# Optimization experiments

Hardware: AMD Instinct MI355X
Metric: run time of the kernel (lower is better)

## Reference

```python
import jax, jax.numpy as jnp
import numpy as np

B, H, S, D = 4, 16, 2048, 64
INV_SCALE_FACTOR = 8.0  # scores are divided by this (== sqrt(D))
DROPOUT_P = 0.0         # deterministic baseline; dropout is identity at p=0


def setup_inputs() -> dict:
    key = jax.random.key(0)
    kq, kk, kv = jax.random.split(key, 3)
    return {
        "query": jax.random.normal(kq, (B, H, S, D), dtype=jnp.float32),
        "key": jax.random.normal(kk, (B, H, S, D), dtype=jnp.float32),
        "value": jax.random.normal(kv, (B, H, S, D), dtype=jnp.float32),
    }


def reference(query, key, value):
    # scores: [B, H, Sq, Sk]
    scores = jnp.einsum("bhqd,bhkd->bhqk", query, key) / INV_SCALE_FACTOR
    probs = jax.nn.softmax(scores, axis=-1)
    # dropout_p == 0.0 -> identity
    out = jnp.einsum("bhqk,bhkd->bhqd", probs, value)
    return out
```

## Files before the change

kernel.cpp:

```cpp
#include <hip/hip_runtime.h>


#define S_LEN 2048
#define D_DIM 64
#define TK    64
#define NTILE (S_LEN / TK)
#define LOG2E_OVER8 0.18033688011112042f
#define VTILE (64 * 64)
#define VBH   (NTILE * VTILE)

typedef __bf16 bf16x8 __attribute__((ext_vector_type(8)));
typedef short  s16x4  __attribute__((ext_vector_type(4)));
typedef float  f32x4  __attribute__((ext_vector_type(4)));
typedef unsigned short us;

__device__ __forceinline__ us f2bf(float f) {
    union { __bf16 h; us u; } c;
    c.h = (__bf16)f;
    return c.u;
}

__device__ __forceinline__ unsigned pk2(float a, float b) {
#if __has_builtin(__builtin_amdgcn_cvt_pk_bf16_f32)
    typedef __bf16 bf2 __attribute__((ext_vector_type(2)));
    union { bf2 h; unsigned u; } c;
    c.h = __builtin_amdgcn_cvt_pk_bf16_f32(a, b);
    return c.u;
#else
    return ((unsigned)f2bf(b) << 16) | f2bf(a);
#endif
}

__device__ __forceinline__ float fast_exp2(float x) {
#if __has_builtin(__builtin_amdgcn_exp2f)
    return __builtin_amdgcn_exp2f(x);
#else
    return exp2f(x);
#endif
}

__device__ __forceinline__ void gload_lds16(const void* g, void* l) {
    __builtin_amdgcn_global_load_lds(
        (const __attribute__((address_space(1))) unsigned int*)g,
        (__attribute__((address_space(3))) unsigned int*)l, 16, 0, 0);
}

__device__ __forceinline__ f32x4 mfma16x16x16(s16x4 a, s16x4 b, f32x4 c) {
#if __has_builtin(__builtin_amdgcn_mfma_f32_16x16x16bf16_1k)
    return __builtin_amdgcn_mfma_f32_16x16x16bf16_1k(a, b, c, 0, 0, 0);
#else
    f32x4 d = c;
    asm volatile("v_mfma_f32_16x16x16_bf16 %0, %1, %2, %0"
                 : "+v"(d) : "v"(a), "v"(b));
    return d;
#endif
}

__global__ __launch_bounds__(256)
void prep(const float* __restrict__ K, const float* __restrict__ V,
          us* __restrict__ Kb, us* __restrict__ Vt) {
    __shared__ us Ls[64 * 68];
    const int bx = blockIdx.x, tid = threadIdx.x;
    if (bx < 4096) {
        const size_t i = ((size_t)bx * 256 + tid) * 8;
        const float4 a = *(const float4*)(K + i);
        const float4 b = *(const float4*)(K + i + 4);
        union { us u[8]; uint4 q; } pk;
        pk.u[0] = f2bf(a.x); pk.u[1] = f2bf(a.y);
        pk.u[2] = f2bf(a.z); pk.u[3] = f2bf(a.w);
        pk.u[4] = f2bf(b.x); pk.u[5] = f2bf(b.y);
        pk.u[6] = f2bf(b.z); pk.u[7] = f2bf(b.w);
        *(uint4*)(Kb + i) = pk.q;
    } else {
        const int idx = bx - 4096;
        const int t = idx & (NTILE - 1), bh = idx >> 5;
        {
            const int r = tid >> 2, seg = tid & 3;
            const float* src = V + ((size_t)bh * S_LEN + t * TK + r) * D_DIM + seg * 16;
            us* dst = &Ls[r * 68 + seg * 16];
#pragma unroll
            for (int i = 0; i < 2; ++i) {
                const float4 v0 = *(const float4*)(src + 8 * i);
                const float4 v1 = *(const float4*)(src + 8 * i + 4);
                union { us u[8]; uint2 q[2]; } pk;
                pk.u[0] = f2bf(v0.x); pk.u[1] = f2bf(v0.y);
                pk.u[2] = f2bf(v0.z); pk.u[3] = f2bf(v0.w);
                pk.u[4] = f2bf(v1.x); pk.u[5] = f2bf(v1.y);
                pk.u[6] = f2bf(v1.z); pk.u[7] = f2bf(v1.w);
                *(uint2*)(dst + 8 * i) = pk.q[0];
                *(uint2*)(dst + 8 * i + 4) = pk.q[1];
            }
        }
        __syncthreads();
        {
            const int lane = tid & 63, db = tid >> 6;
            const int quad = lane >> 4, l15 = lane & 15;
            const int d = db * 16 + l15;
            us* dst = Vt + (size_t)bh * VBH + t * VTILE + lane * 8;
#pragma unroll
            for (int c = 0; c < 2; ++c) {
                union { us u[8]; uint4 q; } pk;
#pragma unroll
                for (int e = 0; e < 8; ++e) {
                    const int k = (2 * c + (e >> 2)) * 16 + quad * 4 + (e & 3);
                    pk.u[e] = Ls[k * 68 + d];
                }
                *(uint4*)(dst + (c * 4 + db) * 512) = pk.q;
            }
        }
    }
}

__global__ __launch_bounds__(256, 4)
void fa_fwd(const float* __restrict__ Qg, const us* __restrict__ Kb,
            const us* __restrict__ Vtb, float* __restrict__ Og) {
    __shared__ __align__(16) us Kl[2][TK * 64];

    const int tid  = threadIdx.x;
    const int w    = tid >> 6;
    const int lane = tid & 63;
    const int l15  = lane & 15;
    const int quad = lane >> 4;
    const int x    = l15 & 7;

    const int bid   = blockIdx.x;
    const int chunk = bid >> 3;
    const int bh    = ((bid & 7) << 3) | (chunk >> 4);
    const int qb    = chunk & 15;
    const size_t base = (size_t)bh * S_LEN * D_DIM;

    bf16x8 bq00, bq01, bq10, bq11;
    {
        const float* q0 = Qg + base + (size_t)(qb * 128 + w * 32 + l15) * D_DIM + quad * 8;
        const float* q1 = q0 + 16 * D_DIM;
#define LOADQ(dst0, dst1, p)                                                  \
        {                                                                     \
            const float4 x0 = *(const float4*)(p);                            \
            const float4 x1 = *(const float4*)((p) + 4);                      \
            const float4 y0 = *(const float4*)((p) + 32);                     \
            const float4 y1 = *(const float4*)((p) + 36);                     \
            dst0[0]=(__bf16)(x0.x*LOG2E_OVER8); dst0[1]=(__bf16)(x0.y*LOG2E_OVER8); \
            dst0[2]=(__bf16)(x0.z*LOG2E_OVER8); dst0[3]=(__bf16)(x0.w*LOG2E_OVER8); \
            dst0[4]=(__bf16)(x1.x*LOG2E_OVER8); dst0[5]=(__bf16)(x1.y*LOG2E_OVER8); \
            dst0[6]=(__bf16)(x1.z*LOG2E_OVER8); dst0[7]=(__bf16)(x1.w*LOG2E_OVER8); \
            dst1[0]=(__bf16)(y0.x*LOG2E_OVER8); dst1[1]=(__bf16)(y0.y*LOG2E_OVER8); \
            dst1[2]=(__bf16)(y0.z*LOG2E_OVER8); dst1[3]=(__bf16)(y0.w*LOG2E_OVER8); \
            dst1[4]=(__bf16)(y1.x*LOG2E_OVER8); dst1[5]=(__bf16)(y1.y*LOG2E_OVER8); \
            dst1[6]=(__bf16)(y1.z*LOG2E_OVER8); dst1[7]=(__bf16)(y1.w*LOG2E_OVER8); \
        }
        LOADQ(bq00, bq01, q0)
        LOADQ(bq10, bq11, q1)
#undef LOADQ
    }

    const int krow   = w * 16 + (lane >> 3);
    const int kchunk = (lane & 7) ^ (lane >> 3);
    const us* ksrc = Kb + base + (size_t)krow * D_DIM + kchunk * 8;
    const us* vg0 = Vtb + (size_t)bh * VBH + lane * 8;

    float lv0 = 0.f, lv1 = 0.f;
    f32x4 oa0[4], oa1[4];
#pragma unroll
    for (int db = 0; db < 4; ++db) {
        oa0[db] = (f32x4){0.f, 0.f, 0.f, 0.f};
        oa1[db] = (f32x4){0.f, 0.f, 0.f, 0.f};
    }

#pragma unroll
    for (int j = 0; j < 2; ++j)
        gload_lds16(ksrc + j * 512, &Kl[0][w * 1024 + j * 512]);
    __syncthreads();

    s16x4 bus0[4], bus1[4];

#define QK_STEP(kb)                                                            \
    {                                                                          \
        const int row_ = (kb) * 16 + l15;                                      \
        const bf16x8 a0 = *(const bf16x8*)&kl[row_ * 64 + ((quad ^ x) * 8)];   \
        const bf16x8 a1 = *(const bf16x8*)&kl[row_ * 64 + (((4 + quad) ^ x) * 8)]; \
        f32x4 c0 = {0.f, 0.f, 0.f, 0.f};                                       \
        c0 = __builtin_amdgcn_mfma_f32_16x16x32_bf16(a0, bq00, c0, 0, 0, 0);   \
        c0 = __builtin_amdgcn_mfma_f32_16x16x32_bf16(a1, bq01, c0, 0, 0, 0);   \
        f32x4 c1 = {0.f, 0.f, 0.f, 0.f};                                       \
        c1 = __builtin_amdgcn_mfma_f32_16x16x32_bf16(a0, bq10, c1, 0, 0, 0);   \
        c1 = __builtin_amdgcn_mfma_f32_16x16x32_bf16(a1, bq11, c1, 0, 0, 0);   \
        const float p00 = fast_exp2(c0[0]), p01 = fast_exp2(c0[1]);            \
        const float p02 = fast_exp2(c0[2]), p03 = fast_exp2(c0[3]);            \
        lv0 += (p00 + p01) + (p02 + p03);                                      \
        const float p10 = fast_exp2(c1[0]), p11 = fast_exp2(c1[1]);            \
        const float p12 = fast_exp2(c1[2]), p13 = fast_exp2(c1[3]);            \
        lv1 += (p10 + p11) + (p12 + p13);                                      \
        union { unsigned u[2]; s16x4 s; } b0_, b1_;                            \
        b0_.u[0] = pk2(p00, p01); b0_.u[1] = pk2(p02, p03);                    \
        b1_.u[0] = pk2(p10, p11); b1_.u[1] = pk2(p12, p13);                    \
        bus0[kb] = b0_.s; bus1[kb] = b1_.s;                                    \
    }

#define PV_PAIR(K0)                                                            \
    _Pragma("unroll")                                                          \
    for (int db = 0; db < 4; ++db) {                                           \
        union { uint4 q; s16x4 s[2]; } va;                                     \
        va.q = vqa[db];                                                        \
        oa0[db] = mfma16x16x16(va.s[0], bus0[K0], oa0[db]);                    \
        oa1[db] = mfma16x16x16(va.s[0], bus1[K0], oa1[db]);                    \
        oa0[db] = mfma16x16x16(va.s[1], bus0[(K0) + 1], oa0[db]);              \
        oa1[db] = mfma16x16x16(va.s[1], bus1[(K0) + 1], oa1[db]);              \
    }

#pragma unroll 1
    for (int t = 0; t < NTILE; ++t) {
        const int cur = t & 1;
        const us* kl = Kl[cur];
        const us* vg = vg0 + (size_t)t * VTILE;

        uint4 vqa[4];
#pragma unroll
        for (int f = 0; f < 4; ++f) vqa[f] = *(const uint4*)(vg + f * 512);

        QK_STEP(0)
        QK_STEP(1)
        PV_PAIR(0)

#pragma unroll
        for (int f = 0; f < 4; ++f) vqa[f] = *(const uint4*)(vg + (4 + f) * 512);

        if (t + 1 < NTILE) {
            const us* ks = ksrc + (size_t)(t + 1) * (TK * D_DIM);
            us* kd = &Kl[cur ^ 1][w * 1024];
#pragma unroll
            for (int j = 0; j < 2; ++j)
                gload_lds16(ks + j * 512, kd + j * 512);
        }

        QK_STEP(2)
        QK_STEP(3)
        PV_PAIR(2)

        __syncthreads();
    }
#undef QK_STEP
#undef PV_PAIR

    float lq0 = lv0;
    lq0 += __shfl_xor(lq0, 16, 64);
    lq0 += __shfl_xor(lq0, 32, 64);
    float lq1 = lv1;
    lq1 += __shfl_xor(lq1, 16, 64);
    lq1 += __shfl_xor(lq1, 32, 64);
    const float inv0 = 1.f / lq0;
    const float inv1 = 1.f / lq1;
    float* op0 = Og + base + (size_t)(qb * 128 + w * 32 + l15) * D_DIM + quad * 4;
    float* op1 = op0 + 16 * D_DIM;
#pragma unroll
    for (int db = 0; db < 4; ++db) {
        float4 v0 = { oa0[db][0] * inv0, oa0[db][1] * inv0,
                      oa0[db][2] * inv0, oa0[db][3] * inv0 };
        *(float4*)(op0 + db * 16) = v0;
        float4 v1 = { oa1[db][0] * inv1, oa1[db][1] * inv1,
                      oa1[db][2] * inv1, oa1[db][3] * inv1 };
        *(float4*)(op1 + db * 16) = v1;
    }
}

extern "C" void kernel_launch(void* const* d_in, const int* in_sizes, int n_in,
                              void* d_out, int out_size, void* d_ws, size_t ws_size,
                              hipStream_t stream) {
    const float* Q = (const float*)d_in[0];
    const float* K = (const float*)d_in[1];
    const float* V = (const float*)d_in[2];
    float* O = (float*)d_out;

    us* Kb = (us*)d_ws;
    us* Vt = Kb + (size_t)64 * S_LEN * D_DIM;

    prep<<<4096 + 2048, 256, 0, stream>>>(K, V, Kb, Vt);
    fa_fwd<<<dim3(1024), 256, 0, stream>>>(Q, Kb, Vt, O);
}
```

Baseline: 212.6 us.

## Software-pipeline QK of next tile with PV of current tile

Restructures the main loop so the QK^T/exp step for tile t+1 is computed while the PV MFMAs for tile t run, using two ping-pong probability register sets and prefetching K two tiles ahead. A prologue computes tile 0 scores and an epilogue finishes the last PV. The aim is to interleave the exp/pack ALU work with MFMA work and hide LDS latency, at the cost of more live registers, which may lower occupancy.

```diff
diff --git a/kernel.cpp b/kernel.cpp
--- a/kernel.cpp
+++ b/kernel.cpp
@@ -166,18 +166,13 @@
         oa1[db] = (f32x4){0.f, 0.f, 0.f, 0.f};
     }
 
-#pragma unroll
-    for (int j = 0; j < 2; ++j)
-        gload_lds16(ksrc + j * 512, &Kl[0][w * 1024 + j * 512]);
-    __syncthreads();
-
-    s16x4 bus0[4], bus1[4];
-
-#define QK_STEP(kb)                                                            \
+    s16x4 busA0[4], busA1[4], busB0[4], busB1[4];
+
+#define QK_STEP(KL, kb, B0, B1)                                                \
     {                                                                          \
         const int row_ = (kb) * 16 + l15;                                      \
-        const bf16x8 a0 = *(const bf16x8*)&kl[row_ * 64 + ((quad ^ x) * 8)];   \
-        const bf16x8 a1 = *(const bf16x8*)&kl[row_ * 64 + (((4 + quad) ^ x) * 8)]; \
+        const bf16x8 a0 = *(const bf16x8*)&(KL)[row_ * 64 + ((quad ^ x) * 8)]; \
+        const bf16x8 a1 = *(const bf16x8*)&(KL)[row_ * 64 + (((4 + quad) ^ x) * 8)]; \
         f32x4 c0 = {0.f, 0.f, 0.f, 0.f};                                       \
         c0 = __builtin_amdgcn_mfma_f32_16x16x32_bf16(a0, bq00, c0, 0, 0, 0);   \
         c0 = __builtin_amdgcn_mfma_f32_16x16x32_bf16(a1, bq01, c0, 0, 0, 0);   \
@@ -193,53 +188,78 @@
         union { unsigned u[2]; s16x4 s; } b0_, b1_;                            \
         b0_.u[0] = pk2(p00, p01); b0_.u[1] = pk2(p02, p03);                    \
         b1_.u[0] = pk2(p10, p11); b1_.u[1] = pk2(p12, p13);                    \
-        bus0[kb] = b0_.s; bus1[kb] = b1_.s;                                    \
-    }
-
-#define PV_PAIR(K0)                                                            \
+        (B0)[kb] = b0_.s; (B1)[kb] = b1_.s;                                    \
+    }
+
+#define PV_PAIR(VQA, B0, B1, K0)                                               \
     _Pragma("unroll")                                                          \
     for (int db = 0; db < 4; ++db) {                                           \
         union { uint4 q; s16x4 s[2]; } va;                                     \
-        va.q = vqa[db];                                                        \
-        oa0[db] = mfma16x16x16(va.s[0], bus0[K0], oa0[db]);                    \
-        oa1[db] = mfma16x16x16(va.s[0], bus1[K0], oa1[db]);                    \
-        oa0[db] = mfma16x16x16(va.s[1], bus0[(K0) + 1], oa0[db]);              \
-        oa1[db] = mfma16x16x16(va.s[1], bus1[(K0) + 1], oa1[db]);              \
-    }
+        va.q = (VQA)[db];                                                      \
+        oa0[db] = mfma16x16x16(va.s[0], (B0)[K0], oa0[db]);                    \
+        oa1[db] = mfma16x16x16(va.s[0], (B1)[K0], oa1[db]);                    \
+        oa0[db] = mfma16x16x16(va.s[1], (B0)[(K0) + 1], oa0[db]);              \
+        oa1[db] = mfma16x16x16(va.s[1], (B1)[(K0) + 1], oa1[db]);              \
+    }
+
+#define TILE_BODY(T, BU0, BU1, BB0, BB1, KLN, KLPF, DOPF)                      \
+    {                                                                          \
+        __syncthreads();                                                       \
+        const us* vg = vg0 + (size_t)(T) * VTILE;                              \
+        uint4 vqa[4];                                                          \
+        _Pragma("unroll")                                                      \
+        for (int f = 0; f < 4; ++f) vqa[f] = *(const uint4*)(vg + f * 512);    \
+        QK_STEP(KLN, 0, BB0, BB1)                                              \
+        QK_STEP(KLN, 1, BB0, BB1)                                              \
+        PV_PAIR(vqa, BU0, BU1, 0)                                              \
+        _Pragma("unroll")                                                      \
+        for (int f = 0; f < 4; ++f) vqa[f] = *(const uint4*)(vg + (4 + f) * 512); \
+        if (DOPF) {                                                            \
+            const us* ks_ = ksrc + (size_t)((T) + 2) * (TK * D_DIM);           \
+            us* kd_ = &(KLPF)[w * 1024];                                       \
+            gload_lds16(ks_, kd_);                                             \
+            gload_lds16(ks_ + 512, kd_ + 512);                                 \
+        }                                                                      \
+        QK_STEP(KLN, 2, BB0, BB1)                                              \
+        QK_STEP(KLN, 3, BB0, BB1)                                              \
+        PV_PAIR(vqa, BU0, BU1, 2)                                              \
+    }
+
+    gload_lds16(ksrc, &Kl[0][w * 1024]);
+    gload_lds16(ksrc + 512, &Kl[0][w * 1024 + 512]);
+    __syncthreads();
+    {
+        const us* ks_ = ksrc + (size_t)(TK * D_DIM);
+        us* kd_ = &Kl[1][w * 1024];
+        gload_lds16(ks_, kd_);
+        gload_lds16(ks_ + 512, kd_ + 512);
+    }
+    QK_STEP(Kl[0], 0, busA0, busA1)
+    QK_STEP(Kl[0], 1, busA0, busA1)
+    QK_STEP(Kl[0], 2, busA0, busA1)
+    QK_STEP(Kl[0], 3, busA0, busA1)
 
 #pragma unroll 1
-    for (int t = 0; t < NTILE; ++t) {
-        const int cur = t & 1;
-        const us* kl = Kl[cur];
-        const us* vg = vg0 + (size_t)t * VTILE;
-
+    for (int it = 0; it < 15; ++it) {
+        const int t0 = it * 2;
+        TILE_BODY(t0,     busA0, busA1, busB0, busB1, Kl[1], Kl[0], 1)
+        TILE_BODY(t0 + 1, busB0, busB1, busA0, busA1, Kl[0], Kl[1], 1)
+    }
+    TILE_BODY(30, busA0, busA1, busB0, busB1, Kl[1], Kl[0], 0)
+
+    {
+        const us* vg = vg0 + (size_t)31 * VTILE;
         uint4 vqa[4];
 #pragma unroll
         for (int f = 0; f < 4; ++f) vqa[f] = *(const uint4*)(vg + f * 512);
-
-        QK_STEP(0)
-        QK_STEP(1)
-        PV_PAIR(0)
-
+        PV_PAIR(vqa, busB0, busB1, 0)
 #pragma unroll
         for (int f = 0; f < 4; ++f) vqa[f] = *(const uint4*)(vg + (4 + f) * 512);
-
-        if (t + 1 < NTILE) {
-            const us* ks = ksrc + (size_t)(t + 1) * (TK * D_DIM);
-            us* kd = &Kl[cur ^ 1][w * 1024];
-#pragma unroll
-            for (int j = 0; j < 2; ++j)
-                gload_lds16(ks + j * 512, kd + j * 512);
-        }
-
-        QK_STEP(2)
-        QK_STEP(3)
-        PV_PAIR(2)
-
-        __syncthreads();
+        PV_PAIR(vqa, busB0, busB1, 2)
     }
 #undef QK_STEP
 #undef PV_PAIR
+#undef TILE_BODY
 
     float lq0 = lv0;
     lq0 += __shfl_xor(lq0, 16, 64);
```

New measurement: 309.8 us. 1.46x slower.

## Software-pipeline K/V tiles across iterations with skewed QK and PV stages

Applied to the files above, without the earlier changes.

Restructures the main loop so the QK score computation for the next tile's first half overlaps with the PV accumulation of the current tile. K is prefetched two tiles ahead into the double buffer, and V register loads are issued one stage early. The loop is manually unrolled by two with a prologue and epilogue. This aims to hide LDS and global load latency behind MFMA work, at the cost of more live registers and more complex barrier placement.

```diff
diff --git a/kernel.cpp b/kernel.cpp
--- a/kernel.cpp
+++ b/kernel.cpp
@@ -166,18 +166,14 @@
         oa1[db] = (f32x4){0.f, 0.f, 0.f, 0.f};
     }
 
-#pragma unroll
-    for (int j = 0; j < 2; ++j)
-        gload_lds16(ksrc + j * 512, &Kl[0][w * 1024 + j * 512]);
-    __syncthreads();
-
     s16x4 bus0[4], bus1[4];
-
-#define QK_STEP(kb)                                                            \
+    uint4 vqa[4];
+
+#define QK_STEP(KL, kb)                                                        \
     {                                                                          \
         const int row_ = (kb) * 16 + l15;                                      \
-        const bf16x8 a0 = *(const bf16x8*)&kl[row_ * 64 + ((quad ^ x) * 8)];   \
-        const bf16x8 a1 = *(const bf16x8*)&kl[row_ * 64 + (((4 + quad) ^ x) * 8)]; \
+        const bf16x8 a0 = *(const bf16x8*)&(KL)[row_ * 64 + ((quad ^ x) * 8)]; \
+        const bf16x8 a1 = *(const bf16x8*)&(KL)[row_ * 64 + (((4 + quad) ^ x) * 8)]; \
         f32x4 c0 = {0.f, 0.f, 0.f, 0.f};                                       \
         c0 = __builtin_amdgcn_mfma_f32_16x16x32_bf16(a0, bq00, c0, 0, 0, 0);   \
         c0 = __builtin_amdgcn_mfma_f32_16x16x32_bf16(a1, bq01, c0, 0, 0, 0);   \
@@ -207,39 +203,60 @@
         oa1[db] = mfma16x16x16(va.s[1], bus1[(K0) + 1], oa1[db]);              \
     }
 
+#define VLOAD(T, F0)                                                           \
+    _Pragma("unroll")                                                          \
+    for (int f = 0; f < 4; ++f)                                                \
+        vqa[f] = *(const uint4*)(vg0 + (size_t)(T) * VTILE + ((F0) + f) * 512);
+
+#define TILE_BODY(T, KLT, KLT1, DOPF)                                          \
+    {                                                                          \
+        QK_STEP(KLT, 2)                                                        \
+        QK_STEP(KLT, 3)                                                        \
+        PV_PAIR(0)                                                             \
+        VLOAD(T, 4)                                                            \
+        __syncthreads();                                                       \
+        if (DOPF) {                                                            \
+            const us* ks_ = ksrc + (size_t)((T) + 2) * (TK * D_DIM);           \
+            us* kd_ = &(KLT)[w * 1024];                                        \
+            gload_lds16(ks_, kd_);                                             \
+            gload_lds16(ks_ + 512, kd_ + 512);                                 \
+        }                                                                      \
+        QK_STEP(KLT1, 0)                                                       \
+        QK_STEP(KLT1, 1)                                                       \
+        PV_PAIR(2)                                                             \
+        VLOAD((T) + 1, 0)                                                      \
+    }
+
+    gload_lds16(ksrc, &Kl[0][w * 1024]);
+    gload_lds16(ksrc + 512, &Kl[0][w * 1024 + 512]);
+    __syncthreads();
+    {
+        const us* ks_ = ksrc + (size_t)(TK * D_DIM);
+        us* kd_ = &Kl[1][w * 1024];
+        gload_lds16(ks_, kd_);
+        gload_lds16(ks_ + 512, kd_ + 512);
+    }
+    QK_STEP(Kl[0], 0)
+    QK_STEP(Kl[0], 1)
+    VLOAD(0, 0)
+
 #pragma unroll 1
-    for (int t = 0; t < NTILE; ++t) {
-        const int cur = t & 1;
-        const us* kl = Kl[cur];
-        const us* vg = vg0 + (size_t)t * VTILE;
-
-        uint4 vqa[4];
-#pragma unroll
-        for (int f = 0; f < 4; ++f) vqa[f] = *(const uint4*)(vg + f * 512);
-
-        QK_STEP(0)
-        QK_STEP(1)
-        PV_PAIR(0)
-
-#pragma unroll
-        for (int f = 0; f < 4; ++f) vqa[f] = *(const uint4*)(vg + (4 + f) * 512);
-
-        if (t + 1 < NTILE) {
-            const us* ks = ksrc + (size_t)(t + 1) * (TK * D_DIM);
-            us* kd = &Kl[cur ^ 1][w * 1024];
-#pragma unroll
-            for (int j = 0; j < 2; ++j)
-                gload_lds16(ks + j * 512, kd + j * 512);
-        }
-
-        QK_STEP(2)
-        QK_STEP(3)
-        PV_PAIR(2)
-
-        __syncthreads();
-    }
+    for (int it = 0; it < 15; ++it) {
+        TILE_BODY(2 * it,     Kl[0], Kl[1], 1)
+        TILE_BODY(2 * it + 1, Kl[1], Kl[0], 1)
+    }
+    TILE_BODY(30, Kl[0], Kl[1], 0)
+
+    QK_STEP(Kl[1], 2)
+    QK_STEP(Kl[1], 3)
+    PV_PAIR(0)
+    VLOAD(31, 4)
+    PV_PAIR(2)
+
 #undef QK_STEP
 #undef PV_PAIR
+#undef VLOAD
+#undef TILE_BODY
 
     float lq0 = lv0;
     lq0 += __shfl_xor(lq0, 16, 64);
```

Result: slower. 341.1 us (+60.5%).

## Pre-swizzle K into MFMA fragment layout and load K directly from global

Applied to the files above, without the earlier changes.

The prep kernel now writes K in a per-lane MFMA fragment order, as it already did for V. The attention kernel then reads K fragments straight from global memory into registers, dropping the LDS double buffer, the async global-to-LDS loads and the per-tile __syncthreads. Occupancy is lowered to 3 blocks per SIMD in launch bounds, giving room for the extra register loads. The risk is higher global and L2 traffic, because each of the four waves fetches the same K tile instead of sharing it through LDS, and less latency hiding without the explicit prefetch.

```diff
diff --git a/kernel.cpp b/kernel.cpp
--- a/kernel.cpp
+++ b/kernel.cpp
@@ -39,12 +39,6 @@
 #endif
 }
 
-__device__ __forceinline__ void gload_lds16(const void* g, void* l) {
-    __builtin_amdgcn_global_load_lds(
-        (const __attribute__((address_space(1))) unsigned int*)g,
-        (__attribute__((address_space(3))) unsigned int*)l, 16, 0, 0);
-}
-
 __device__ __forceinline__ f32x4 mfma16x16x16(s16x4 a, s16x4 b, f32x4 c) {
 #if __has_builtin(__builtin_amdgcn_mfma_f32_16x16x16bf16_1k)
     return __builtin_amdgcn_mfma_f32_16x16x16bf16_1k(a, b, c, 0, 0, 0);
@@ -58,70 +52,70 @@
 
 __global__ __launch_bounds__(256)
 void prep(const float* __restrict__ K, const float* __restrict__ V,
-          us* __restrict__ Kb, us* __restrict__ Vt) {
+          us* __restrict__ Kt, us* __restrict__ Vt) {
     __shared__ us Ls[64 * 68];
     const int bx = blockIdx.x, tid = threadIdx.x;
-    if (bx < 4096) {
-        const size_t i = ((size_t)bx * 256 + tid) * 8;
-        const float4 a = *(const float4*)(K + i);
-        const float4 b = *(const float4*)(K + i + 4);
-        union { us u[8]; uint4 q; } pk;
-        pk.u[0] = f2bf(a.x); pk.u[1] = f2bf(a.y);
-        pk.u[2] = f2bf(a.z); pk.u[3] = f2bf(a.w);
-        pk.u[4] = f2bf(b.x); pk.u[5] = f2bf(b.y);
-        pk.u[6] = f2bf(b.z); pk.u[7] = f2bf(b.w);
-        *(uint4*)(Kb + i) = pk.q;
+    const bool isV = bx < 2048;
+    const int idx = isV ? bx : bx - 2048;
+    const int t = idx & (NTILE - 1), bh = idx >> 5;
+    {
+        const float* sb = isV ? V : K;
+        const int r = tid >> 2, seg = tid & 3;
+        const float* src = sb + ((size_t)bh * S_LEN + t * TK + r) * D_DIM + seg * 16;
+        us* dst = &Ls[r * 68 + seg * 16];
+#pragma unroll
+        for (int i = 0; i < 2; ++i) {
+            const float4 v0 = *(const float4*)(src + 8 * i);
+            const float4 v1 = *(const float4*)(src + 8 * i + 4);
+            union { us u[8]; uint2 q[2]; } pk;
+            pk.u[0] = f2bf(v0.x); pk.u[1] = f2bf(v0.y);
+            pk.u[2] = f2bf(v0.z); pk.u[3] = f2bf(v0.w);
+            pk.u[4] = f2bf(v1.x); pk.u[5] = f2bf(v1.y);
+            pk.u[6] = f2bf(v1.z); pk.u[7] = f2bf(v1.w);
+            *(uint2*)(dst + 8 * i) = pk.q[0];
+            *(uint2*)(dst + 8 * i + 4) = pk.q[1];
+        }
+    }
+    __syncthreads();
+    if (isV) {
+        const int lane = tid & 63, db = tid >> 6;
+        const int quad = lane >> 4, l15 = lane & 15;
+        const int d = db * 16 + l15;
+        us* dst = Vt + (size_t)bh * VBH + t * VTILE + lane * 8;
+#pragma unroll
+        for (int c = 0; c < 2; ++c) {
+            union { us u[8]; uint4 q; } pk;
+#pragma unroll
+            for (int e = 0; e < 8; ++e) {
+                const int k = (2 * c + (e >> 2)) * 16 + quad * 4 + (e & 3);
+                pk.u[e] = Ls[k * 68 + d];
+            }
+            *(uint4*)(dst + (c * 4 + db) * 512) = pk.q;
+        }
     } else {
-        const int idx = bx - 4096;
-        const int t = idx & (NTILE - 1), bh = idx >> 5;
-        {
-            const int r = tid >> 2, seg = tid & 3;
-            const float* src = V + ((size_t)bh * S_LEN + t * TK + r) * D_DIM + seg * 16;
-            us* dst = &Ls[r * 68 + seg * 16];
-#pragma unroll
-            for (int i = 0; i < 2; ++i) {
-                const float4 v0 = *(const float4*)(src + 8 * i);
-                const float4 v1 = *(const float4*)(src + 8 * i + 4);
-                union { us u[8]; uint2 q[2]; } pk;
-                pk.u[0] = f2bf(v0.x); pk.u[1] = f2bf(v0.y);
-                pk.u[2] = f2bf(v0.z); pk.u[3] = f2bf(v0.w);
-                pk.u[4] = f2bf(v1.x); pk.u[5] = f2bf(v1.y);
-                pk.u[6] = f2bf(v1.z); pk.u[7] = f2bf(v1.w);
-                *(uint2*)(dst + 8 * i) = pk.q[0];
-                *(uint2*)(dst + 8 * i + 4) = pk.q[1];
-            }
-        }
-        __syncthreads();
-        {
-            const int lane = tid & 63, db = tid >> 6;
-            const int quad = lane >> 4, l15 = lane & 15;
-            const int d = db * 16 + l15;
-            us* dst = Vt + (size_t)bh * VBH + t * VTILE + lane * 8;
-#pragma unroll
-            for (int c = 0; c < 2; ++c) {
-                union { us u[8]; uint4 q; } pk;
-#pragma unroll
-                for (int e = 0; e < 8; ++e) {
-                    const int k = (2 * c + (e >> 2)) * 16 + quad * 4 + (e & 3);
-                    pk.u[e] = Ls[k * 68 + d];
-                }
-                *(uint4*)(dst + (c * 4 + db) * 512) = pk.q;
-            }
-        }
-    }
-}
-
-__global__ __launch_bounds__(256, 4)
-void fa_fwd(const float* __restrict__ Qg, const us* __restrict__ Kb,
+        const int lane = tid & 63, fhi = tid >> 6;
+        const int quad = lane >> 4, l15 = lane & 15;
+        const int row = fhi * 16 + l15;
+        us* dst = Kt + (size_t)bh * VBH + t * VTILE + lane * 8;
+        union { us u[8]; uint4 q; } p0, p1;
+#pragma unroll
+        for (int e = 0; e < 8; ++e) {
+            p0.u[e] = Ls[row * 68 + quad * 8 + e];
+            p1.u[e] = Ls[row * 68 + (quad + 4) * 8 + e];
+        }
+        *(uint4*)(dst + (2 * fhi) * 512) = p0.q;
+        *(uint4*)(dst + (2 * fhi + 1) * 512) = p1.q;
+    }
+}
+
+__global__ __launch_bounds__(256, 3)
+void fa_fwd(const float* __restrict__ Qg, const us* __restrict__ Ktb,
             const us* __restrict__ Vtb, float* __restrict__ Og) {
-    __shared__ __align__(16) us Kl[2][TK * 64];
-
     const int tid  = threadIdx.x;
     const int w    = tid >> 6;
     const int lane = tid & 63;
     const int l15  = lane & 15;
     const int quad = lane >> 4;
-    const int x    = l15 & 7;
 
     const int bid   = blockIdx.x;
     const int chunk = bid >> 3;
@@ -153,9 +147,7 @@
 #undef LOADQ
     }
 
-    const int krow   = w * 16 + (lane >> 3);
-    const int kchunk = (lane & 7) ^ (lane >> 3);
-    const us* ksrc = Kb + base + (size_t)krow * D_DIM + kchunk * 8;
+    const us* kg0 = Ktb + (size_t)bh * VBH + lane * 8;
     const us* vg0 = Vtb + (size_t)bh * VBH + lane * 8;
 
     float lv0 = 0.f, lv1 = 0.f;
@@ -166,24 +158,18 @@
         oa1[db] = (f32x4){0.f, 0.f, 0.f, 0.f};
     }
 
-#pragma unroll
-    for (int j = 0; j < 2; ++j)
-        gload_lds16(ksrc + j * 512, &Kl[0][w * 1024 + j * 512]);
-    __syncthreads();
-
     s16x4 bus0[4], bus1[4];
 
-#define QK_STEP(kb)                                                            \
+#define QK_STEP(kb, KA, KB)                                                    \
     {                                                                          \
-        const int row_ = (kb) * 16 + l15;                                      \
-        const bf16x8 a0 = *(const bf16x8*)&kl[row_ * 64 + ((quad ^ x) * 8)];   \
-        const bf16x8 a1 = *(const bf16x8*)&kl[row_ * 64 + (((4 + quad) ^ x) * 8)]; \
+        union { uint4 q; bf16x8 h; } aU, bU;                                   \
+        aU.q = (KA); bU.q = (KB);                                              \
         f32x4 c0 = {0.f, 0.f, 0.f, 0.f};                                       \
-        c0 = __builtin_amdgcn_mfma_f32_16x16x32_bf16(a0, bq00, c0, 0, 0, 0);   \
-        c0 = __builtin_amdgcn_mfma_f32_16x16x32_bf16(a1, bq01, c0, 0, 0, 0);   \
+        c0 = __builtin_amdgcn_mfma_f32_16x16x32_bf16(aU.h, bq00, c0, 0, 0, 0); \
+        c0 = __builtin_amdgcn_mfma_f32_16x16x32_bf16(bU.h, bq01, c0, 0, 0, 0); \
         f32x4 c1 = {0.f, 0.f, 0.f, 0.f};                                       \
-        c1 = __builtin_amdgcn_mfma_f32_16x16x32_bf16(a0, bq10, c1, 0, 0, 0);   \
-        c1 = __builtin_amdgcn_mfma_f32_16x16x32_bf16(a1, bq11, c1, 0, 0, 0);   \
+        c1 = __builtin_amdgcn_mfma_f32_16x16x32_bf16(aU.h, bq10, c1, 0, 0, 0); \
+        c1 = __builtin_amdgcn_mfma_f32_16x16x32_bf16(bU.h, bq11, c1, 0, 0, 0); \
         const float p00 = fast_exp2(c0[0]), p01 = fast_exp2(c0[1]);            \
         const float p02 = fast_exp2(c0[2]), p03 = fast_exp2(c0[3]);            \
         lv0 += (p00 + p01) + (p02 + p03);                                      \
@@ -196,50 +182,46 @@
         bus0[kb] = b0_.s; bus1[kb] = b1_.s;                                    \
     }
 
-#define PV_PAIR(K0)                                                            \
-    _Pragma("unroll")                                                          \
-    for (int db = 0; db < 4; ++db) {                                           \
+#define PV_ONE(VQ, DB, K0)                                                     \
+    {                                                                          \
         union { uint4 q; s16x4 s[2]; } va;                                     \
-        va.q = vqa[db];                                                        \
-        oa0[db] = mfma16x16x16(va.s[0], bus0[K0], oa0[db]);                    \
-        oa1[db] = mfma16x16x16(va.s[0], bus1[K0], oa1[db]);                    \
-        oa0[db] = mfma16x16x16(va.s[1], bus0[(K0) + 1], oa0[db]);              \
-        oa1[db] = mfma16x16x16(va.s[1], bus1[(K0) + 1], oa1[db]);              \
+        va.q = (VQ);                                                           \
+        oa0[DB] = mfma16x16x16(va.s[0], bus0[K0], oa0[DB]);                    \
+        oa1[DB] = mfma16x16x16(va.s[0], bus1[K0], oa1[DB]);                    \
+        oa0[DB] = mfma16x16x16(va.s[1], bus0[(K0) + 1], oa0[DB]);              \
+        oa1[DB] = mfma16x16x16(va.s[1], bus1[(K0) + 1], oa1[DB]);              \
     }
 
 #pragma unroll 1
     for (int t = 0; t < NTILE; ++t) {
-        const int cur = t & 1;
-        const us* kl = Kl[cur];
+        const us* kg = kg0 + (size_t)t * VTILE;
         const us* vg = vg0 + (size_t)t * VTILE;
 
-        uint4 vqa[4];
-#pragma unroll
-        for (int f = 0; f < 4; ++f) vqa[f] = *(const uint4*)(vg + f * 512);
-
-        QK_STEP(0)
-        QK_STEP(1)
-        PV_PAIR(0)
-
-#pragma unroll
-        for (int f = 0; f < 4; ++f) vqa[f] = *(const uint4*)(vg + (4 + f) * 512);
-
-        if (t + 1 < NTILE) {
-            const us* ks = ksrc + (size_t)(t + 1) * (TK * D_DIM);
-            us* kd = &Kl[cur ^ 1][w * 1024];
-#pragma unroll
-            for (int j = 0; j < 2; ++j)
-                gload_lds16(ks + j * 512, kd + j * 512);
-        }
-
-        QK_STEP(2)
-        QK_STEP(3)
-        PV_PAIR(2)
-
-        __syncthreads();
+        const uint4 k0 = *(const uint4*)(kg);
+        const uint4 k1 = *(const uint4*)(kg + 512);
+        const uint4 k2 = *(const uint4*)(kg + 1024);
+        const uint4 k3 = *(const uint4*)(kg + 1536);
+        const uint4 v0 = *(const uint4*)(vg);
+        const uint4 v1 = *(const uint4*)(vg + 512);
+        const uint4 v2 = *(const uint4*)(vg + 1024);
+        const uint4 v3 = *(const uint4*)(vg + 1536);
+        QK_STEP(0, k0, k1)
+        QK_STEP(1, k2, k3)
+        const uint4 k4 = *(const uint4*)(kg + 2048);
+        const uint4 k5 = *(const uint4*)(kg + 2560);
+        const uint4 k6 = *(const uint4*)(kg + 3072);
+        const uint4 k7 = *(const uint4*)(kg + 3584);
+        PV_ONE(v0, 0, 0) PV_ONE(v1, 1, 0) PV_ONE(v2, 2, 0) PV_ONE(v3, 3, 0)
+        const uint4 v4 = *(const uint4*)(vg + 2048);
+        const uint4 v5 = *(const uint4*)(vg + 2560);
+        const uint4 v6 = *(const uint4*)(vg + 3072);
+        const uint4 v7 = *(const uint4*)(vg + 3584);
+        QK_STEP(2, k4, k5)
+        QK_STEP(3, k6, k7)
+        PV_ONE(v4, 0, 2) PV_ONE(v5, 1, 2) PV_ONE(v6, 2, 2) PV_ONE(v7, 3, 2)
     }
 #undef QK_STEP
-#undef PV_PAIR
+#undef PV_ONE
 
     float lq0 = lv0;
     lq0 += __shfl_xor(lq0, 16, 64);
@@ -270,9 +252,9 @@
     const float* V = (const float*)d_in[2];
     float* O = (float*)d_out;
 
-    us* Kb = (us*)d_ws;
-    us* Vt = Kb + (size_t)64 * S_LEN * D_DIM;
-
-    prep<<<4096 + 2048, 256, 0, stream>>>(K, V, Kb, Vt);
-    fa_fwd<<<dim3(1024), 256, 0, stream>>>(Q, Kb, Vt, O);
-}
+    us* Kt = (us*)d_ws;
+    us* Vt = Kt + (size_t)64 * VBH;
+
+    prep<<<4096, 256, 0, stream>>>(K, V, Kt, Vt);
+    fa_fwd<<<dim3(1024), 256, 0, stream>>>(Q, Kt, Vt, O);
+}
```

Result: no change. 214.9 us (+1.1%).
